# Kernel optimization log

Hardware: AMD Instinct MI355X
Metric: run time of the kernel (lower is better)

## Reference

```python
import jax, jax.numpy as jnp
import numpy as np

K_MASK = -2.3819763e+38
NUM_KV_HEADS = 4
SOFT_CAP = 50.0
WINDOW = 1024
ROPE_BASE = 10000.0
ROPE_SCALE = 1.0


def rms_norm(x, scale=None, eps=1e-6):
    var = jnp.mean(jnp.square(x), axis=-1, keepdims=True)
    normed = x * jax.lax.rsqrt(var + eps)
    if scale is not None:
        normed = normed * (1.0 + scale)
    return normed


def apply_rope(x, positions):
    # x: [B, T, N, H], positions: [B, T]
    head_dim = x.shape[-1]
    fraction = 2.0 * jnp.arange(head_dim // 2, dtype=jnp.float32) / head_dim
    timescale = ROPE_BASE ** fraction  # [H/2]
    sinusoid = positions[..., None, None].astype(jnp.float32) / timescale / ROPE_SCALE  # [B,T,1,H/2]
    sin, cos = jnp.sin(sinusoid), jnp.cos(sinusoid)
    first, second = jnp.split(x, 2, axis=-1)
    return jnp.concatenate([first * cos - second * sin,
                            second * cos + first * sin], axis=-1).astype(x.dtype)


def setup_inputs() -> dict:
    key = jax.random.key(0)
    ks = jax.random.split(key, 8)
    B, T, D, N, K, H, F = 2, 2048, 2048, 8, NUM_KV_HEADS, 256, 8192
    CACHE = 4096
    x = jax.random.normal(ks[0], (B, T, D), dtype=jnp.float32)
    segment_pos = jnp.broadcast_to(jnp.arange(T, dtype=jnp.int32)[None, :], (B, T))
    # causal mask over cache slots: after scatter, slot s (< T) holds position s; slots >= T are empty
    s_idx = jnp.arange(CACHE)
    t_idx = jnp.arange(T)
    attn_mask = (s_idx[None, :] <= t_idx[:, None]) & (s_idx[None, :] < T)
    attn_mask = jnp.broadcast_to(attn_mask[None], (B, T, CACHE))
    cache_k = jnp.zeros((B, CACHE, K, H), dtype=jnp.float32)
    cache_v = jnp.zeros((B, CACHE, K, H), dtype=jnp.float32)
    cache_positions = jnp.zeros((B, CACHE), dtype=jnp.int32)
    end_index = jnp.zeros((B,), dtype=jnp.int32)
    w_q = jax.random.normal(ks[1], (N, D, H), dtype=jnp.float32) * 0.02
    w_kv = jax.random.normal(ks[2], (2, K, D, H), dtype=jnp.float32) * 0.02
    w_attn_vec = jax.random.normal(ks[3], (N, H, D), dtype=jnp.float32) * 0.02
    w_gating = jax.random.normal(ks[4], (2, F, D), dtype=jnp.float32) * 0.02
    w_linear = jax.random.normal(ks[5], (F, D), dtype=jnp.float32) * 0.02
    return {
        'x': x, 'segment_pos': segment_pos, 'attn_mask': attn_mask,
        'cache_k': cache_k, 'cache_v': cache_v,
        'cache_positions': cache_positions, 'end_index': end_index,
        'w_q': w_q, 'w_kv': w_kv, 'w_attn_vec': w_attn_vec,
        'q_norm_scale': jnp.zeros((H,), dtype=jnp.float32),
        'k_norm_scale': jnp.zeros((H,), dtype=jnp.float32),
        'pre_attn_scale': jnp.zeros((D,), dtype=jnp.float32),
        'post_attn_scale': jnp.zeros((D,), dtype=jnp.float32),
        'pre_ffw_scale': jnp.zeros((D,), dtype=jnp.float32),
        'post_ffw_scale': jnp.zeros((D,), dtype=jnp.float32),
        'w_gating': w_gating, 'w_linear': w_linear,
        'skip_scale': jnp.ones((1,), dtype=jnp.float32),
    }


def reference(x, segment_pos, attn_mask, cache_k, cache_v, cache_positions, end_index,
              w_q, w_kv, w_attn_vec, q_norm_scale, k_norm_scale,
              pre_attn_scale, post_attn_scale, pre_ffw_scale, post_ffw_scale,
              w_gating, w_linear, skip_scale):
    B, T, D = x.shape
    cache_size = cache_v.shape[1]

    h = rms_norm(x, pre_attn_scale)

    # --- attention ---
    q = jnp.einsum('BTD,NDH->BTNH', h, w_q)
    q = rms_norm(q, q_norm_scale)
    q = apply_rope(q, segment_pos)

    k, v = jnp.einsum('BSD,CKDH->CBSKH', h, w_kv)
    k = rms_norm(k, k_norm_scale)
    v = rms_norm(v, None)
    k = apply_rope(k, segment_pos)

    # KV-cache scatter (ring-buffer indexing)
    idx = (end_index[:, None] + jnp.arange(T)[None, :]) % cache_size  # [B,T]
    bidx = jnp.arange(B)[:, None]
    v = cache_v.at[bidx, idx].set(v)              # [B,S,K,H]
    k = cache_k.at[bidx, idx].set(k)
    cache_pos = cache_positions.at[bidx, idx].set(segment_pos)  # [B,S]

    # GQA logits
    N, H = q.shape[2], q.shape[3]
    G = N // NUM_KV_HEADS
    qg = q.reshape(B, T, NUM_KV_HEADS, G, H)
    logits = jnp.einsum('BTKGH,BSKH->BTKGS', qg, k).reshape(B, T, N, cache_size)

    # soft cap
    logits = jnp.tanh(logits / SOFT_CAP) * SOFT_CAP

    # sliding-window mask against cache positions
    sliding = (cache_pos[:, None, :] > segment_pos[:, :, None] - WINDOW) & \
              (cache_pos[:, None, :] < segment_pos[:, :, None] + WINDOW)  # [B,T,S]
    mask = attn_mask & sliding

    padded = jnp.where(mask[:, :, None, :], logits, K_MASK)
    probs = jax.nn.softmax(padded, axis=-1).astype(k.dtype)

    pg = probs.reshape(B, T, NUM_KV_HEADS, G, cache_size)
    encoded = jnp.einsum('BTKGS,BSKH->BTKGH', pg, v).reshape(B, T, N, H)
    attn_out = jnp.einsum('BTNH,NHD->BTD', encoded, w_attn_vec)

    # post-attn norm + residual (skip_scale on the skip connection)
    attn_out = rms_norm(attn_out, post_attn_scale)
    attn_out = x * skip_scale + attn_out

    # --- feed-forward ---
    ffw_in = rms_norm(attn_out, pre_ffw_scale)
    gate = jnp.einsum('BTF,CHF->BTCH', ffw_in, w_gating)  # C=2
    act = jax.nn.gelu(gate[..., 0, :]) * gate[..., 1, :]
    ffw_out = jnp.einsum('BTH,HF->BTF', act, w_linear)
    ffw_out = rms_norm(ffw_out, post_ffw_scale)

    return attn_out + ffw_out
```

## Files before the change

kernel.cpp:

```cpp
#include <hip/hip_runtime.h>


typedef _Float16 h8 __attribute__((ext_vector_type(8)));
typedef _Float16 h4 __attribute__((ext_vector_type(4)));
typedef float f4 __attribute__((ext_vector_type(4)));

#define BDIM 2
#define TDIM 2048
#define DDIM 2048
#define NQ 8
#define NKV 4
#define HDIM 256
#define FDIM 8192
#define MROWS (BDIM * TDIM)
#define WINDOW 1024
#define QS 4096

#define BAR() asm volatile("s_barrier" ::: "memory")

__device__ __forceinline__ float gelu_fast(float x) {
  float u = 1.5957691216057308f * (x + 0.044715f * x * x * x);
  float e = __expf(u);
  return x * e / (e + 1.f);
}

__device__ __forceinline__ void g2l16(const _Float16* g, _Float16* l) {
  __builtin_amdgcn_global_load_lds(
      (const __attribute__((address_space(1))) void*)g,
      (__attribute__((address_space(3))) void*)l, 16, 0, 0);
}

__device__ inline float block_sum(float v, float* sbuf) {
#pragma unroll
  for (int off = 32; off; off >>= 1) v += __shfl_xor(v, off, 64);
  __syncthreads();
  if ((threadIdx.x & 63) == 0) sbuf[threadIdx.x >> 6] = v;
  __syncthreads();
  return sbuf[0] + sbuf[1] + sbuf[2] + sbuf[3];
}

template <int EPI>
__global__ __launch_bounds__(512, 2) void gemm256(
    const _Float16* __restrict__ A, const _Float16* __restrict__ Bt,
    void* __restrict__ Cout, int M, int Nc, int K) {
  __shared__ _Float16 As[3][256 * 64];
  __shared__ _Float16 Bs[3][128 * 64];
  (void)M;
  const int tid = threadIdx.x;
  const int lane = tid & 63, w = tid >> 6;
  const int nwg = gridDim.x;
  const int bid2 = (blockIdx.x & 7) * (nwg >> 3) + (blockIdx.x >> 3);
  const int nbx = Nc >> 7;
  const int bx = bid2 % nbx, by = bid2 / nbx;
  const int m0 = by * 256, n0 = bx * 128;
  const int wm = (w >> 1) * 64, wn = (w & 1) * 64;
  const int l16 = lane & 15, quad = lane >> 4;

  const int lr = lane >> 3;
  const int swz8 = ((lane & 7) ^ lr) << 3;
  const _Float16* Ag = A + (size_t)(m0 + w * 32 + lr) * K + swz8;
  const _Float16* Bg = Bt + (size_t)(n0 + w * 16 + lr) * K + swz8;

  const int qs8 = (quad ^ (l16 & 3)) << 3;
  const int kxo = ((l16 >> 2) & 1) << 5;
  int aoff[4], boff[4];
#pragma unroll
  for (int i = 0; i < 4; i++) {
    aoff[i] = (wm + i * 16 + l16) * 64 + qs8;
    boff[i] = (wn + i * 16 + l16) * 64 + qs8;
  }

  f4 acc[4][4];
#pragma unroll
  for (int i = 0; i < 4; i++)
#pragma unroll
    for (int j = 0; j < 4; j++) {
      acc[i][j][0] = 0.f; acc[i][j][1] = 0.f; acc[i][j][2] = 0.f; acc[i][j][3] = 0.f;
    }

#define SA(b, kt, c) g2l16(Ag + (size_t)(c) * 8 * K + (size_t)(kt) * 64, \
                           &As[b][(w * 32 + (c) * 8) * 64])
#define SB(b, kt, c) g2l16(Bg + (size_t)(c) * 8 * K + (size_t)(kt) * 64, \
                           &Bs[b][(w * 16 + (c) * 8) * 64])

  SA(0, 0, 0); SA(0, 0, 1); SA(0, 0, 2); SA(0, 0, 3); SB(0, 0, 0); SB(0, 0, 1);
  SA(1, 1, 0); SA(1, 1, 1); SA(1, 1, 2); SA(1, 1, 3); SB(1, 1, 0); SB(1, 1, 1);
  asm volatile("s_waitcnt vmcnt(6)" ::: "memory");
  BAR();

  const int nt = K >> 6;
  for (int kt = 0; kt < nt; ++kt) {
    const int cur = kt % 3, nb = (kt + 2) % 3;
    const bool pf = (kt + 2) < nt;
    const _Float16* Ab = As[cur];
    const _Float16* Bb = Bs[cur];
    h8 af[4][2], bf[4][2];
#pragma unroll
    for (int i = 0; i < 4; i++) {
      af[i][0] = *(const h8*)&Ab[aoff[i] + kxo];
      af[i][1] = *(const h8*)&Ab[aoff[i] + (kxo ^ 32)];
    }
#pragma unroll
    for (int i = 0; i < 2; i++) {
      bf[i][0] = *(const h8*)&Bb[boff[i] + kxo];
      bf[i][1] = *(const h8*)&Bb[boff[i] + (kxo ^ 32)];
    }
    if (pf) { SA(nb, kt + 2, 0); SA(nb, kt + 2, 1); SA(nb, kt + 2, 2); }
    BAR();
    __builtin_amdgcn_s_setprio(1);
#pragma unroll
    for (int mi = 0; mi < 4; mi++)
#pragma unroll
      for (int ni = 0; ni < 2; ni++)
#pragma unroll
        for (int ks = 0; ks < 2; ks++)
          acc[mi][ni] = __builtin_amdgcn_mfma_f32_16x16x32_f16(
              af[mi][ks], bf[ni][ks], acc[mi][ni], 0, 0, 0);
    __builtin_amdgcn_s_setprio(0);
    BAR();
#pragma unroll
    for (int i = 2; i < 4; i++) {
      bf[i][0] = *(const h8*)&Bb[boff[i] + kxo];
      bf[i][1] = *(const h8*)&Bb[boff[i] + (kxo ^ 32)];
    }
    if (pf) { SA(nb, kt + 2, 3); SB(nb, kt + 2, 0); SB(nb, kt + 2, 1); }
    BAR();
    __builtin_amdgcn_s_setprio(1);
#pragma unroll
    for (int mi = 0; mi < 4; mi++)
#pragma unroll
      for (int ni = 2; ni < 4; ni++)
#pragma unroll
        for (int ks = 0; ks < 2; ks++)
          acc[mi][ni] = __builtin_amdgcn_mfma_f32_16x16x32_f16(
              af[mi][ks], bf[ni][ks], acc[mi][ni], 0, 0, 0);
    __builtin_amdgcn_s_setprio(0);
    if (pf)                 asm volatile("s_waitcnt vmcnt(6)" ::: "memory");
    else if (kt + 2 == nt)  asm volatile("s_waitcnt vmcnt(0)" ::: "memory");
    BAR();
  }
#undef SA
#undef SB

#pragma unroll
  for (int mi = 0; mi < 4; mi++)
#pragma unroll
    for (int ni = 0; ni < 4; ni++)
#pragma unroll
      for (int r = 0; r < 4; r++) {
        const int rg = m0 + wm + mi * 16 + quad * 4 + r;
        const int cg = n0 + wn + ni * 16 + l16;
        const size_t idx = (size_t)rg * Nc + cg;
        if (EPI == 0) ((float*)Cout)[idx] = acc[mi][ni][r];
        else          ((_Float16*)Cout)[idx] = (_Float16)acc[mi][ni][r];
      }
}

__global__ __launch_bounds__(512, 2) void gemm_gate256(
    const _Float16* __restrict__ A, const _Float16* __restrict__ B0,
    const _Float16* __restrict__ B1, _Float16* __restrict__ act,
    int M, int Nc, int K) {
  __shared__ _Float16 As[2][256 * 64];
  __shared__ _Float16 B0s[2][128 * 64];
  __shared__ _Float16 B1s[2][128 * 64];
  const int tid = threadIdx.x;
  const int lane = tid & 63, w = tid >> 6;
  const int nwg = gridDim.x;
  const int bid2 = (blockIdx.x & 7) * (nwg >> 3) + (blockIdx.x >> 3);
  const int nby = M >> 8;
  const int by = bid2 % nby, bx = bid2 / nby;
  const int m0 = by * 256, n0 = bx * 128;
  const int wm = (w >> 1) * 64, wn = (w & 1) * 64;
  const int l16 = lane & 15, quad = lane >> 4;

  const int lr = lane >> 3;
  const int swz8 = ((lane & 7) ^ lr) << 3;
  const _Float16* Ag  = A  + (size_t)(m0 + w * 32 + lr) * K + swz8;
  const _Float16* B0g = B0 + (size_t)(n0 + w * 16 + lr) * K + swz8;
  const _Float16* B1g = B1 + (size_t)(n0 + w * 16 + lr) * K + swz8;

  const int qs8 = (quad ^ (l16 & 3)) << 3;
  const int kxo = ((l16 >> 2) & 1) << 5;
  int aoff[4], boff[4];
#pragma unroll
  for (int i = 0; i < 4; i++) {
    aoff[i] = (wm + i * 16 + l16) * 64 + qs8;
    boff[i] = (wn + i * 16 + l16) * 64 + qs8;
  }

  f4 acc0[4][4], acc1[4][4];
#pragma unroll
  for (int i = 0; i < 4; i++)
#pragma unroll
    for (int j = 0; j < 4; j++) {
      acc0[i][j][0] = 0.f; acc0[i][j][1] = 0.f; acc0[i][j][2] = 0.f; acc0[i][j][3] = 0.f;
      acc1[i][j][0] = 0.f; acc1[i][j][1] = 0.f; acc1[i][j][2] = 0.f; acc1[i][j][3] = 0.f;
    }

#define SA(b, kt, c)  g2l16(Ag  + (size_t)(c) * 8 * K + (size_t)(kt) * 64, \
                            &As[b][(w * 32 + (c) * 8) * 64])
#define SB0(b, kt, c) g2l16(B0g + (size_t)(c) * 8 * K + (size_t)(kt) * 64, \
                            &B0s[b][(w * 16 + (c) * 8) * 64])
#define SB1(b, kt, c) g2l16(B1g + (size_t)(c) * 8 * K + (size_t)(kt) * 64, \
                            &B1s[b][(w * 16 + (c) * 8) * 64])

  SA(0, 0, 0); SA(0, 0, 1); SA(0, 0, 2); SA(0, 0, 3);
  SB0(0, 0, 0); SB0(0, 0, 1); SB1(0, 0, 0); SB1(0, 0, 1);
  asm volatile("s_waitcnt vmcnt(0)" ::: "memory");
  BAR();

  const int nt = K >> 6;
  for (int kt = 0; kt < nt; ++kt) {
    const int cur = kt & 1, nb = cur ^ 1;
    const bool pf = (kt + 1) < nt;
    const _Float16* Ab  = As[cur];
    const _Float16* Bb0 = B0s[cur];
    const _Float16* Bb1 = B1s[cur];
    h8 af[4][2], b0f[4][2], b1f[4][2];
#pragma unroll
    for (int i = 0; i < 4; i++) {
      af[i][0] = *(const h8*)&Ab[aoff[i] + kxo];
      af[i][1] = *(const h8*)&Ab[aoff[i] + (kxo ^ 32)];
    }
#pragma unroll
    for (int i = 0; i < 4; i++) {
      b0f[i][0] = *(const h8*)&Bb0[boff[i] + kxo];
      b0f[i][1] = *(const h8*)&Bb0[boff[i] + (kxo ^ 32)];
    }
    if (pf) {
      SA(nb, kt + 1, 0); SA(nb, kt + 1, 1); SA(nb, kt + 1, 2); SA(nb, kt + 1, 3);
      SB0(nb, kt + 1, 0); SB0(nb, kt + 1, 1);
      SB1(nb, kt + 1, 0); SB1(nb, kt + 1, 1);
    }
    BAR();
    __builtin_amdgcn_s_setprio(1);
#pragma unroll
    for (int mi = 0; mi < 4; mi++)
#pragma unroll
      for (int ni = 0; ni < 4; ni++)
#pragma unroll
        for (int ks = 0; ks < 2; ks++)
          acc0[mi][ni] = __builtin_amdgcn_mfma_f32_16x16x32_f16(
              af[mi][ks], b0f[ni][ks], acc0[mi][ni], 0, 0, 0);
    __builtin_amdgcn_s_setprio(0);
    BAR();
#pragma unroll
    for (int i = 0; i < 4; i++) {
      b1f[i][0] = *(const h8*)&Bb1[boff[i] + kxo];
      b1f[i][1] = *(const h8*)&Bb1[boff[i] + (kxo ^ 32)];
    }
    BAR();
    __builtin_amdgcn_s_setprio(1);
#pragma unroll
    for (int mi = 0; mi < 4; mi++)
#pragma unroll
      for (int ni = 0; ni < 4; ni++)
#pragma unroll
        for (int ks = 0; ks < 2; ks++)
          acc1[mi][ni] = __builtin_amdgcn_mfma_f32_16x16x32_f16(
              af[mi][ks], b1f[ni][ks], acc1[mi][ni], 0, 0, 0);
    __builtin_amdgcn_s_setprio(0);
    if (pf) asm volatile("s_waitcnt vmcnt(0)" ::: "memory");
    BAR();
  }
#undef SA
#undef SB0
#undef SB1

#pragma unroll
  for (int mi = 0; mi < 4; mi++)
#pragma unroll
    for (int ni = 0; ni < 4; ni++)
#pragma unroll
      for (int r = 0; r < 4; r++) {
        const int rg = m0 + wm + mi * 16 + quad * 4 + r;
        const int cg = n0 + wn + ni * 16 + l16;
        act[(size_t)rg * Nc + cg] =
            (_Float16)(gelu_fast(acc0[mi][ni][r]) * acc1[mi][ni][r]);
      }
}

__global__ __launch_bounds__(256) void transpose_cast_kernel(
    const float* __restrict__ in, _Float16* __restrict__ out,
    int R, int C, size_t in_zstride, size_t out_zstride) {
  __shared__ float tile[64][65];
  const float* ip = in + blockIdx.z * in_zstride;
  _Float16* op = out + blockIdx.z * out_zstride;
  const int cb = blockIdx.x * 64, rb = blockIdx.y * 64;
  const int tx = threadIdx.x & 15, ty = threadIdx.x >> 4;
#pragma unroll
  for (int i = 0; i < 4; i++) {
    f4 v = *(const f4*)&ip[(size_t)(rb + ty + 16 * i) * C + cb + tx * 4];
    tile[ty + 16 * i][tx * 4 + 0] = v[0];
    tile[ty + 16 * i][tx * 4 + 1] = v[1];
    tile[ty + 16 * i][tx * 4 + 2] = v[2];
    tile[ty + 16 * i][tx * 4 + 3] = v[3];
  }
  __syncthreads();
#pragma unroll
  for (int i = 0; i < 4; i++) {
    const int c = ty + 16 * i;
    h4 o;
#pragma unroll
    for (int j = 0; j < 4; j++) o[j] = (_Float16)tile[tx * 4 + j][c];
    *(h4*)&op[(size_t)(cb + c) * R + rb + tx * 4] = o;
  }
}

__global__ void cast_fp16_kernel(const float* __restrict__ in,
                                 _Float16* __restrict__ out, int n4) {
  int i = blockIdx.x * 256 + threadIdx.x;
  if (i < n4) {
    f4 v = ((const f4*)in)[i];
    h4 o;
    o[0] = (_Float16)v[0]; o[1] = (_Float16)v[1];
    o[2] = (_Float16)v[2]; o[3] = (_Float16)v[3];
    ((h4*)out)[i] = o;
  }
}

__global__ __launch_bounds__(256) void rmsnorm_fp16_kernel(
    const float* __restrict__ in, const float* __restrict__ scale,
    _Float16* __restrict__ out) {
  __shared__ float sbuf[4];
  const int row = blockIdx.x, tid = threadIdx.x;
  const float* r = in + (size_t)row * 2048;
  f4 a = ((const f4*)r)[tid];
  f4 b = ((const f4*)r)[tid + 256];
  float ss = a[0]*a[0] + a[1]*a[1] + a[2]*a[2] + a[3]*a[3] +
             b[0]*b[0] + b[1]*b[1] + b[2]*b[2] + b[3]*b[3];
  float tot = block_sum(ss, sbuf);
  float rs = rsqrtf(tot * (1.f / 2048.f) + 1e-6f);
  f4 s0 = ((const f4*)scale)[tid];
  f4 s1 = ((const f4*)scale)[tid + 256];
  h4 o0, o1;
#pragma unroll
  for (int j = 0; j < 4; j++) {
    o0[j] = (_Float16)(a[j] * rs * (1.f + s0[j]));
    o1[j] = (_Float16)(b[j] * rs * (1.f + s1[j]));
  }
  ((h4*)(out + (size_t)row * 2048))[tid] = o0;
  ((h4*)(out + (size_t)row * 2048))[tid + 256] = o1;
}

__global__ __launch_bounds__(256) void headnorm_qkv_kernel(
    const _Float16* __restrict__ qkv, _Float16* __restrict__ out,
    const float* __restrict__ qsc, const float* __restrict__ ksc,
    const int* __restrict__ pos_arr) {
  const int inst = blockIdx.x * 4 + (threadIdx.x >> 6);
  const int lane = threadIdx.x & 63;
  const int row = inst >> 4, slot = inst & 15;
  const _Float16* r = qkv + (size_t)row * QS + slot * 256;
  h4 vh = ((const h4*)r)[lane];
  f4 v;
#pragma unroll
  for (int j = 0; j < 4; j++) v[j] = (float)vh[j];
  float ss = v[0]*v[0] + v[1]*v[1] + v[2]*v[2] + v[3]*v[3];
#pragma unroll
  for (int off = 32; off; off >>= 1) ss += __shfl_xor(ss, off, 64);
  const float rs = rsqrtf(ss * (1.f / 256.f) + 1e-6f);
  const float* scale = (slot < 8) ? qsc : (slot < 12 ? ksc : nullptr);
  f4 nv;
  if (scale) {
    f4 sc = ((const f4*)scale)[lane];
#pragma unroll
    for (int j = 0; j < 4; j++) nv[j] = v[j] * rs * (1.f + sc[j]);
  } else {
#pragma unroll
    for (int j = 0; j < 4; j++) nv[j] = v[j] * rs;
  }
  h4 res;
  if (slot < 12) {
    const float pos = (float)pos_arr[row];
    const bool lo = lane < 32;
#pragma unroll
    for (int j = 0; j < 4; j++) {
      float partner = __shfl_xor(nv[j], 32, 64);
      const int ph = (lane * 4 + j) & 127;
      float it = exp2f((float)ph * -0.103810253f);
      float ang = pos * it;
      float sn, cs;
      sincosf(ang, &sn, &cs);
      res[j] = (_Float16)(lo ? (nv[j] * cs - partner * sn)
                             : (nv[j] * cs + partner * sn));
    }
  } else {
#pragma unroll
    for (int j = 0; j < 4; j++) res[j] = (_Float16)nv[j];
  }
  ((h4*)(out + (size_t)row * QS + slot * 256))[lane] = res;
}

__global__ __launch_bounds__(256) void transpose_v_kernel(
    const _Float16* __restrict__ qkvh, _Float16* __restrict__ vT) {
  __shared__ _Float16 tile[32][33];
  const int z = blockIdx.z;
  const int b = z >> 2, kvh = z & 3;
  const int tb = blockIdx.x * 32, hb = blockIdx.y * 32;
  const int x = threadIdx.x, y = threadIdx.y;
#pragma unroll
  for (int i = 0; i < 4; i++)
    tile[y + 8 * i][x] =
        qkvh[(size_t)(b * TDIM + tb + y + 8 * i) * QS + 3072 + kvh * 256 + hb + x];
  __syncthreads();
#pragma unroll
  for (int i = 0; i < 4; i++)
    vT[((size_t)z * HDIM + hb + y + 8 * i) * TDIM + tb + x] = tile[x][y + 8 * i];
}

__global__ __launch_bounds__(256) void attn_kernel(
    const _Float16* __restrict__ qkvh, const _Float16* __restrict__ vT,
    _Float16* __restrict__ enc) {
  __shared__ _Float16 Ks[32 * 256];
  __shared__ _Float16 Vs[256 * 32];
  __shared__ _Float16 Ps[4][16 * 32];
  const int t0 = blockIdx.x * 64;
  const int n = blockIdx.y;
  const int b = blockIdx.z;
  const int kvh = n >> 1;
  const int tid = threadIdx.x;
  const int w = tid >> 6, lane = tid & 63, l16 = lane & 15, quad = lane >> 4;
  const int kxr = (l16 >> 2) & 1;
  const int qsK8 = (quad ^ (l16 & 3)) << 3;
  const int qsV8 = (quad ^ ((l16 >> 1) & 3)) << 3;

  h8 qfrag[8];
  {
    const int trow = t0 + w * 16 + l16;
    const _Float16* qp =
        qkvh + (size_t)(b * TDIM + trow) * QS + n * HDIM + quad * 8;
#pragma unroll
    for (int ks = 0; ks < 8; ks++) qfrag[ks] = *(const h8*)(qp + ks * 32);
  }

  f4 O[16];
#pragma unroll
  for (int i = 0; i < 16; i++) { O[i][0] = 0.f; O[i][1] = 0.f; O[i][2] = 0.f; O[i][3] = 0.f; }
  float m_i[4], l_i[4];
#pragma unroll
  for (int r = 0; r < 4; r++) { m_i[r] = -1e30f; l_i[r] = 0.f; }

  int s_begin = t0 - (WINDOW - 1);
  if (s_begin < 0) s_begin = 0;
  s_begin &= ~31;
  const int s_end = t0 + 64;
  const _Float16* kbase = qkvh + (size_t)b * TDIM * QS + 2048 + kvh * HDIM;
  const _Float16* vbase = vT + ((size_t)(b * NKV + kvh) * HDIM) * TDIM;

  for (int s0 = s_begin; s0 < s_end; s0 += 32) {
    __syncthreads();
#pragma unroll
    for (int p = 0; p < 4; p++) {
      int g = p * 256 + tid;
      {
        int si = g >> 5, c = g & 31;
        *(h8*)&Ks[si * 256 + ((c ^ (si & 7)) << 3)] =
            *(const h8*)(kbase + (size_t)(s0 + si) * QS + (c << 3));
      }
      {
        int h = g >> 2, c = g & 3;
        *(h8*)&Vs[h * 32 + ((c ^ ((g >> 3) & 3)) << 3)] =
            *(const h8*)(vbase + (size_t)h * TDIM + s0 + (c << 3));
      }
    }
    __syncthreads();

    float P[2][4], cmax[4];
#pragma unroll
    for (int r = 0; r < 4; r++) cmax[r] = -1e30f;
#pragma unroll
    for (int sc = 0; sc < 2; sc++) {
      f4 lg; lg[0] = 0.f; lg[1] = 0.f; lg[2] = 0.f; lg[3] = 0.f;
#pragma unroll
      for (int ks = 0; ks < 8; ks++) {
        h8 kb = *(const h8*)&Ks[(sc * 16 + l16) * 256 + ((ks ^ kxr) << 5) + qsK8];
        lg = __builtin_amdgcn_mfma_f32_16x16x32_f16(qfrag[ks], kb, lg, 0, 0, 0);
      }
      const int scol = s0 + sc * 16 + l16;
#pragma unroll
      for (int r = 0; r < 4; r++) {
        const int trow = t0 + w * 16 + quad * 4 + r;
        float t = __expf(lg[r] * 0.04f);
        float xv = 50.f - 100.f * __builtin_amdgcn_rcpf(t + 1.f);
        bool valid = (scol <= trow) && (scol > trow - WINDOW);
        P[sc][r] = valid ? xv : -1e30f;
        cmax[r] = fmaxf(cmax[r], P[sc][r]);
      }
    }
#pragma unroll
    for (int off = 1; off < 16; off <<= 1)
#pragma unroll
      for (int r = 0; r < 4; r++) cmax[r] = fmaxf(cmax[r], __shfl_xor(cmax[r], off, 16));
    float alpha[4], psum[4];
#pragma unroll
    for (int r = 0; r < 4; r++) {
      float mnew = fmaxf(m_i[r], cmax[r]);
      alpha[r] = __expf(m_i[r] - mnew);
      m_i[r] = mnew;
      psum[r] = 0.f;
    }
#pragma unroll
    for (int sc = 0; sc < 2; sc++)
#pragma unroll
      for (int r = 0; r < 4; r++) {
        float pv = __expf(P[sc][r] - m_i[r]);
        P[sc][r] = pv;
        psum[r] += pv;
      }
#pragma unroll
    for (int off = 1; off < 16; off <<= 1)
#pragma unroll
      for (int r = 0; r < 4; r++) psum[r] += __shfl_xor(psum[r], off, 16);
#pragma unroll
    for (int r = 0; r < 4; r++) l_i[r] = l_i[r] * alpha[r] + psum[r];
#pragma unroll
    for (int i = 0; i < 16; i++)
#pragma unroll
      for (int r = 0; r < 4; r++) O[i][r] *= alpha[r];
#pragma unroll
    for (int sc = 0; sc < 2; sc++)
#pragma unroll
      for (int r = 0; r < 4; r++)
        Ps[w][(quad * 4 + r) * 32 + sc * 16 + l16] = (_Float16)P[sc][r];
    h8 pa = *(const h8*)&Ps[w][l16 * 32 + quad * 8];
#pragma unroll
    for (int ht = 0; ht < 16; ht++) {
      h8 vb = *(const h8*)&Vs[(ht * 16 + l16) * 32 + qsV8];
      O[ht] = __builtin_amdgcn_mfma_f32_16x16x32_f16(pa, vb, O[ht], 0, 0, 0);
    }
  }

  float invl[4];
#pragma unroll
  for (int r = 0; r < 4; r++) invl[r] = 1.f / l_i[r];
#pragma unroll
  for (int ht = 0; ht < 16; ht++)
#pragma unroll
    for (int r = 0; r < 4; r++) {
      const int trow = t0 + w * 16 + quad * 4 + r;
      enc[((size_t)(b * TDIM + trow)) * (NQ * HDIM) + n * HDIM + ht * 16 + l16] =
          (_Float16)(O[ht][r] * invl[r]);
    }
}

__global__ __launch_bounds__(256) void postattn_kernel(
    const float* __restrict__ attnraw, const float* __restrict__ x,
    const float* __restrict__ post_scale, const float* __restrict__ pre_ffw_scale,
    const float* __restrict__ skip, float* __restrict__ attn_out,
    _Float16* __restrict__ ffw_in) {
  __shared__ float sbuf[4];
  const int row = blockIdx.x, tid = threadIdx.x;
  const float* ar = attnraw + (size_t)row * 2048;
  const float* xr = x + (size_t)row * 2048;
  f4 a0 = ((const f4*)ar)[tid], a1 = ((const f4*)ar)[tid + 256];
  float ss = a0[0]*a0[0] + a0[1]*a0[1] + a0[2]*a0[2] + a0[3]*a0[3] +
             a1[0]*a1[0] + a1[1]*a1[1] + a1[2]*a1[2] + a1[3]*a1[3];
  float tot = block_sum(ss, sbuf);
  float rs = rsqrtf(tot * (1.f / 2048.f) + 1e-6f);
  const float sk = skip[0];
  f4 x0 = ((const f4*)xr)[tid], x1 = ((const f4*)xr)[tid + 256];
  f4 p0 = ((const f4*)post_scale)[tid], p1 = ((const f4*)post_scale)[tid + 256];
  f4 at0, at1;
#pragma unroll
  for (int j = 0; j < 4; j++) {
    at0[j] = x0[j] * sk + a0[j] * rs * (1.f + p0[j]);
    at1[j] = x1[j] * sk + a1[j] * rs * (1.f + p1[j]);
  }
  ((f4*)(attn_out + (size_t)row * 2048))[tid] = at0;
  ((f4*)(attn_out + (size_t)row * 2048))[tid + 256] = at1;
  float ss2 = at0[0]*at0[0] + at0[1]*at0[1] + at0[2]*at0[2] + at0[3]*at0[3] +
              at1[0]*at1[0] + at1[1]*at1[1] + at1[2]*at1[2] + at1[3]*at1[3];
  float tot2 = block_sum(ss2, sbuf);
  float rs2 = rsqrtf(tot2 * (1.f / 2048.f) + 1e-6f);
  f4 f0 = ((const f4*)pre_ffw_scale)[tid], f1 = ((const f4*)pre_ffw_scale)[tid + 256];
  h4 o0, o1;
#pragma unroll
  for (int j = 0; j < 4; j++) {
    o0[j] = (_Float16)(at0[j] * rs2 * (1.f + f0[j]));
    o1[j] = (_Float16)(at1[j] * rs2 * (1.f + f1[j]));
  }
  ((h4*)(ffw_in + (size_t)row * 2048))[tid] = o0;
  ((h4*)(ffw_in + (size_t)row * 2048))[tid + 256] = o1;
}

__global__ __launch_bounds__(256) void final_kernel(
    const _Float16* __restrict__ ffw, const float* __restrict__ attn_out,
    const float* __restrict__ post_ffw_scale, float* __restrict__ out) {
  __shared__ float sbuf[4];
  const int row = blockIdx.x, tid = threadIdx.x;
  const _Float16* fr = ffw + (size_t)row * 2048;
  const float* ar = attn_out + (size_t)row * 2048;
  h4 fh0 = ((const h4*)fr)[tid], fh1 = ((const h4*)fr)[tid + 256];
  f4 a0, a1;
#pragma unroll
  for (int j = 0; j < 4; j++) { a0[j] = (float)fh0[j]; a1[j] = (float)fh1[j]; }
  float ss = a0[0]*a0[0] + a0[1]*a0[1] + a0[2]*a0[2] + a0[3]*a0[3] +
             a1[0]*a1[0] + a1[1]*a1[1] + a1[2]*a1[2] + a1[3]*a1[3];
  float tot = block_sum(ss, sbuf);
  float rs = rsqrtf(tot * (1.f / 2048.f) + 1e-6f);
  f4 s0 = ((const f4*)post_ffw_scale)[tid], s1 = ((const f4*)post_ffw_scale)[tid + 256];
  f4 x0 = ((const f4*)ar)[tid], x1 = ((const f4*)ar)[tid + 256];
  f4 o0, o1;
#pragma unroll
  for (int j = 0; j < 4; j++) {
    o0[j] = x0[j] + a0[j] * rs * (1.f + s0[j]);
    o1[j] = x1[j] + a1[j] * rs * (1.f + s1[j]);
  }
  ((f4*)(out + (size_t)row * 2048))[tid] = o0;
  ((f4*)(out + (size_t)row * 2048))[tid + 256] = o1;
}

extern "C" void kernel_launch(void* const* d_in, const int* in_sizes, int n_in,
                              void* d_out, int out_size, void* d_ws, size_t ws_size,
                              hipStream_t stream) {
  (void)in_sizes; (void)n_in; (void)out_size; (void)ws_size;
  const float* x              = (const float*)d_in[0];
  const int*   segment_pos    = (const int*)d_in[1];
  const float* w_q            = (const float*)d_in[7];
  const float* w_kv           = (const float*)d_in[8];
  const float* w_attn_vec     = (const float*)d_in[9];
  const float* q_norm_scale   = (const float*)d_in[10];
  const float* k_norm_scale   = (const float*)d_in[11];
  const float* pre_attn_scale = (const float*)d_in[12];
  const float* post_attn_scale= (const float*)d_in[13];
  const float* pre_ffw_scale  = (const float*)d_in[14];
  const float* post_ffw_scale = (const float*)d_in[15];
  const float* w_gating       = (const float*)d_in[16];
  const float* w_linear       = (const float*)d_in[17];
  const float* skip_scale     = (const float*)d_in[18];

  char* ws = (char*)d_ws;
  const size_t MB = 1024 * 1024;
  _Float16* Wqkv  = (_Float16*)(ws + 0);
  _Float16* Wo    = (_Float16*)(ws + 0);
  _Float16* Wg    = (_Float16*)(ws + 0);
  _Float16* Wl    = (_Float16*)(ws + 0);
  _Float16* Hbf   = (_Float16*)(ws + 64 * MB);
  float* attnF    = (float*)(ws + 80 * MB);
  _Float16* qkvraw= (_Float16*)(ws + 112 * MB);
  _Float16* qkvh  = (_Float16*)(ws + 144 * MB);
  _Float16* enc   = (_Float16*)(ws + 176 * MB);
  float* attnraw  = (float*)(ws + 192 * MB);
  _Float16* vT    = (_Float16*)(ws + 224 * MB);
  _Float16* act   = (_Float16*)(ws + 112 * MB);
  _Float16* ffw   = (_Float16*)(ws + 192 * MB);
  float* outp     = (float*)d_out;

  transpose_cast_kernel<<<dim3(HDIM / 64, DDIM / 64, NQ), 256, 0, stream>>>(
      w_q, Wqkv, DDIM, HDIM, (size_t)DDIM * HDIM, (size_t)HDIM * DDIM);
  transpose_cast_kernel<<<dim3(HDIM / 64, DDIM / 64, NKV), 256, 0, stream>>>(
      w_kv, Wqkv + (size_t)2048 * DDIM, DDIM, HDIM,
      (size_t)DDIM * HDIM, (size_t)HDIM * DDIM);
  transpose_cast_kernel<<<dim3(HDIM / 64, DDIM / 64, NKV), 256, 0, stream>>>(
      w_kv + (size_t)NKV * DDIM * HDIM, Wqkv + (size_t)3072 * DDIM, DDIM, HDIM,
      (size_t)DDIM * HDIM, (size_t)HDIM * DDIM);
  rmsnorm_fp16_kernel<<<MROWS, 256, 0, stream>>>(x, pre_attn_scale, Hbf);
  gemm256<1><<<dim3((QS / 128) * (MROWS / 256)), 512, 0, stream>>>(
      Hbf, Wqkv, qkvraw, MROWS, QS, DDIM);
  headnorm_qkv_kernel<<<(MROWS * 16) / 4, 256, 0, stream>>>(
      qkvraw, qkvh, q_norm_scale, k_norm_scale, segment_pos);
  transpose_v_kernel<<<dim3(TDIM / 32, HDIM / 32, BDIM * NKV), dim3(32, 8), 0, stream>>>(
      qkvh, vT);
  attn_kernel<<<dim3(TDIM / 64, NQ, BDIM), 256, 0, stream>>>(qkvh, vT, enc);
  transpose_cast_kernel<<<dim3(DDIM / 64, (NQ * HDIM) / 64, 1), 256, 0, stream>>>(
      w_attn_vec, Wo, NQ * HDIM, DDIM, 0, 0);
  gemm256<0><<<dim3((DDIM / 128) * (MROWS / 256)), 512, 0, stream>>>(
      enc, Wo, attnraw, MROWS, DDIM, NQ * HDIM);
  postattn_kernel<<<MROWS, 256, 0, stream>>>(attnraw, x, post_attn_scale,
                                             pre_ffw_scale, skip_scale, attnF, Hbf);
  cast_fp16_kernel<<<(2 * FDIM * DDIM / 4 + 255) / 256, 256, 0, stream>>>(
      w_gating, Wg, 2 * FDIM * DDIM / 4);
  gemm_gate256<<<dim3((FDIM / 128) * (MROWS / 256)), 512, 0, stream>>>(
      Hbf, Wg, Wg + (size_t)FDIM * DDIM, act, MROWS, FDIM, DDIM);
  transpose_cast_kernel<<<dim3(DDIM / 64, FDIM / 64, 1), 256, 0, stream>>>(
      w_linear, Wl, FDIM, DDIM, 0, 0);
  gemm256<1><<<dim3((DDIM / 128) * (MROWS / 256)), 512, 0, stream>>>(
      act, Wl, ffw, MROWS, DDIM, FDIM);
  final_kernel<<<MROWS, 256, 0, stream>>>(ffw, attnF, post_ffw_scale, outp);
}
```

Before: 1.147 ms.

## Triple-buffer A tiles and interleave prefetches across four MFMA phases in gate GEMM

The fused gate/up GEMM now keeps three shared-memory buffers for the A tile, so A is prefetched two k-steps ahead while B stays double-buffered. Global-to-LDS loads are spread across four smaller MFMA phases, and partial vmcnt waits replace a full drain. This is meant to hide global load latency behind compute. The extra LDS forces launch bounds down to one workgroup per CU, which reduces occupancy. It also adds more barriers per iteration.

```diff
diff --git a/kernel.cpp b/kernel.cpp
--- a/kernel.cpp
+++ b/kernel.cpp
@@ -156,11 +156,11 @@
       }
 }
 
-__global__ __launch_bounds__(512, 2) void gemm_gate256(
+__global__ __launch_bounds__(512, 1) void gemm_gate256(
     const _Float16* __restrict__ A, const _Float16* __restrict__ B0,
     const _Float16* __restrict__ B1, _Float16* __restrict__ act,
     int M, int Nc, int K) {
-  __shared__ _Float16 As[2][256 * 64];
+  __shared__ _Float16 As[3][256 * 64];
   __shared__ _Float16 B0s[2][128 * 64];
   __shared__ _Float16 B1s[2][128 * 64];
   const int tid = threadIdx.x;
@@ -206,16 +206,19 @@
 
   SA(0, 0, 0); SA(0, 0, 1); SA(0, 0, 2); SA(0, 0, 3);
   SB0(0, 0, 0); SB0(0, 0, 1); SB1(0, 0, 0); SB1(0, 0, 1);
-  asm volatile("s_waitcnt vmcnt(0)" ::: "memory");
+  SA(1, 1, 0); SA(1, 1, 1); SA(1, 1, 2); SA(1, 1, 3);
+  asm volatile("s_waitcnt vmcnt(4)" ::: "memory");
   BAR();
 
   const int nt = K >> 6;
   for (int kt = 0; kt < nt; ++kt) {
-    const int cur = kt & 1, nb = cur ^ 1;
-    const bool pf = (kt + 1) < nt;
-    const _Float16* Ab  = As[cur];
-    const _Float16* Bb0 = B0s[cur];
-    const _Float16* Bb1 = B1s[cur];
+    const int ca = kt % 3, na = (kt + 2) % 3;
+    const int cb = kt & 1, nbb = (kt + 1) & 1;
+    const bool pfA = (kt + 2) < nt;
+    const bool pfB = (kt + 1) < nt;
+    const _Float16* Ab  = As[ca];
+    const _Float16* Bb0 = B0s[cb];
+    const _Float16* Bb1 = B1s[cb];
     h8 af[4][2], b0f[4][2], b1f[4][2];
 #pragma unroll
     for (int i = 0; i < 4; i++) {
@@ -223,21 +226,17 @@
       af[i][1] = *(const h8*)&Ab[aoff[i] + (kxo ^ 32)];
     }
 #pragma unroll
-    for (int i = 0; i < 4; i++) {
+    for (int i = 0; i < 2; i++) {
       b0f[i][0] = *(const h8*)&Bb0[boff[i] + kxo];
       b0f[i][1] = *(const h8*)&Bb0[boff[i] + (kxo ^ 32)];
     }
-    if (pf) {
-      SA(nb, kt + 1, 0); SA(nb, kt + 1, 1); SA(nb, kt + 1, 2); SA(nb, kt + 1, 3);
-      SB0(nb, kt + 1, 0); SB0(nb, kt + 1, 1);
-      SB1(nb, kt + 1, 0); SB1(nb, kt + 1, 1);
-    }
+    if (pfB) { SB0(nbb, kt + 1, 0); SB0(nbb, kt + 1, 1); }
     BAR();
     __builtin_amdgcn_s_setprio(1);
 #pragma unroll
     for (int mi = 0; mi < 4; mi++)
 #pragma unroll
-      for (int ni = 0; ni < 4; ni++)
+      for (int ni = 0; ni < 2; ni++)
 #pragma unroll
         for (int ks = 0; ks < 2; ks++)
           acc0[mi][ni] = __builtin_amdgcn_mfma_f32_16x16x32_f16(
@@ -245,22 +244,60 @@
     __builtin_amdgcn_s_setprio(0);
     BAR();
 #pragma unroll
-    for (int i = 0; i < 4; i++) {
+    for (int i = 2; i < 4; i++) {
+      b0f[i][0] = *(const h8*)&Bb0[boff[i] + kxo];
+      b0f[i][1] = *(const h8*)&Bb0[boff[i] + (kxo ^ 32)];
+    }
+    if (pfB) { SB1(nbb, kt + 1, 0); SB1(nbb, kt + 1, 1); }
+    BAR();
+    __builtin_amdgcn_s_setprio(1);
+#pragma unroll
+    for (int mi = 0; mi < 4; mi++)
+#pragma unroll
+      for (int ni = 2; ni < 4; ni++)
+#pragma unroll
+        for (int ks = 0; ks < 2; ks++)
+          acc0[mi][ni] = __builtin_amdgcn_mfma_f32_16x16x32_f16(
+              af[mi][ks], b0f[ni][ks], acc0[mi][ni], 0, 0, 0);
+    __builtin_amdgcn_s_setprio(0);
+    BAR();
+#pragma unroll
+    for (int i = 0; i < 2; i++) {
       b1f[i][0] = *(const h8*)&Bb1[boff[i] + kxo];
       b1f[i][1] = *(const h8*)&Bb1[boff[i] + (kxo ^ 32)];
     }
+    if (pfA) { SA(na, kt + 2, 0); SA(na, kt + 2, 1); }
     BAR();
     __builtin_amdgcn_s_setprio(1);
 #pragma unroll
     for (int mi = 0; mi < 4; mi++)
 #pragma unroll
-      for (int ni = 0; ni < 4; ni++)
+      for (int ni = 0; ni < 2; ni++)
 #pragma unroll
         for (int ks = 0; ks < 2; ks++)
           acc1[mi][ni] = __builtin_amdgcn_mfma_f32_16x16x32_f16(
               af[mi][ks], b1f[ni][ks], acc1[mi][ni], 0, 0, 0);
     __builtin_amdgcn_s_setprio(0);
-    if (pf) asm volatile("s_waitcnt vmcnt(0)" ::: "memory");
+    BAR();
+#pragma unroll
+    for (int i = 2; i < 4; i++) {
+      b1f[i][0] = *(const h8*)&Bb1[boff[i] + kxo];
+      b1f[i][1] = *(const h8*)&Bb1[boff[i] + (kxo ^ 32)];
+    }
+    if (pfA) { SA(na, kt + 2, 2); SA(na, kt + 2, 3); }
+    BAR();
+    __builtin_amdgcn_s_setprio(1);
+#pragma unroll
+    for (int mi = 0; mi < 4; mi++)
+#pragma unroll
+      for (int ni = 2; ni < 4; ni++)
+#pragma unroll
+        for (int ks = 0; ks < 2; ks++)
+          acc1[mi][ni] = __builtin_amdgcn_mfma_f32_16x16x32_f16(
+              af[mi][ks], b1f[ni][ks], acc1[mi][ni], 0, 0, 0);
+    __builtin_amdgcn_s_setprio(0);
+    if (pfA)      asm volatile("s_waitcnt vmcnt(4)" ::: "memory");
+    else if (pfB) asm volatile("s_waitcnt vmcnt(0)" ::: "memory");
     BAR();
   }
 #undef SA
```

Result: faster. 1.086 ms (-5.3%).
